# Kernel optimization log

Hardware: AMD Instinct MI355X
Metric: run time of the kernel (lower is better)

Reference implementation:

```python
import jax, jax.numpy as jnp
import numpy as np

DIM = 1024
HEADS = 16
DIM_HEAD = 64


def setup_inputs() -> dict:
    key = jax.random.key(0)
    ks = jax.random.split(key, 6)
    b, n = 2, 2048
    x = jax.random.normal(ks[0], (b, n, DIM), dtype=jnp.float32)
    gamma = jnp.ones((DIM,), dtype=jnp.float32)
    w_qkv = jax.random.normal(ks[1], (DIM, 3 * HEADS * DIM_HEAD), dtype=jnp.float32) * (DIM ** -0.5)
    w_gates = jax.random.normal(ks[2], (DIM, HEADS), dtype=jnp.float32) * (DIM ** -0.5)
    b_gates = jnp.zeros((HEADS,), dtype=jnp.float32)
    w_out = jax.random.normal(ks[3], (HEADS * DIM_HEAD, DIM), dtype=jnp.float32) * ((HEADS * DIM_HEAD) ** -0.5)
    freqs = jax.random.uniform(ks[4], (DIM_HEAD // 2,), dtype=jnp.float32)
    return {"x": x, "gamma": gamma, "w_qkv": w_qkv, "w_gates": w_gates,
            "b_gates": b_gates, "w_out": w_out, "freqs": freqs}


def _rotate_half(t):
    # interleaved pairs: (x1, x2) -> (-x2, x1)
    tp = t.reshape(t.shape[:-1] + (t.shape[-1] // 2, 2))
    x1, x2 = tp[..., 0], tp[..., 1]
    return jnp.stack((-x2, x1), axis=-1).reshape(t.shape)


def reference(x, gamma, w_qkv, w_gates, b_gates, w_out, freqs):
    b, n, d = x.shape
    # RMSNorm variant: divide by L2 norm, scale by gamma * sqrt(dim)
    xn = x / jnp.linalg.norm(x, axis=-1, keepdims=True)
    xn = xn * gamma * (d ** 0.5)
    # QKV projection: (b, n, 3*H*D) -> q,k,v each (b, h, n, dh)
    qkv = xn @ w_qkv
    qkv = qkv.reshape(b, n, 3, HEADS, DIM_HEAD).transpose(2, 0, 3, 1, 4)
    q, k, v = qkv[0], qkv[1], qkv[2]
    # Inline RoPE (interleaved): freqs (n, dh)
    pos = jnp.arange(n, dtype=freqs.dtype)
    f = jnp.repeat(pos[:, None] * freqs[None, :], 2, axis=-1)  # (n, dh)
    cos_f, sin_f = jnp.cos(f), jnp.sin(f)
    q = q * cos_f + _rotate_half(q) * sin_f
    k = k * cos_f + _rotate_half(k) * sin_f
    # SDPA
    scale = DIM_HEAD ** -0.5
    scores = jnp.einsum('bhqd,bhkd->bhqk', q, k) * scale
    attn = jax.nn.softmax(scores, axis=-1)
    out = jnp.einsum('bhqk,bhkd->bhqd', attn, v)  # (b, h, n, dh)
    # per-head sigmoid gate from normalized input
    gates = xn @ w_gates + b_gates  # (b, n, h)
    out = out * jax.nn.sigmoid(gates.transpose(0, 2, 1))[..., None]
    # merge heads and output projection
    out = out.transpose(0, 2, 1, 3).reshape(b, n, HEADS * DIM_HEAD)
    return out @ w_out
```

## Files before the change

kernel.cpp:

```cpp
#include <hip/hip_runtime.h>

typedef __bf16 bf16_t;
typedef __bf16 bf16x8 __attribute__((ext_vector_type(8)));
typedef __bf16 bf16x4 __attribute__((ext_vector_type(4)));
typedef float f32x4 __attribute__((ext_vector_type(4)));

#define B_  2
#define N_  2048
#define D_  1024
#define H_  16
#define DH_ 64

#define QSCALE 0.18033688011112042f
#define NEGC  -11.541560327111707f

#if __has_builtin(__builtin_amdgcn_exp2f)
#define EXP2F(x) __builtin_amdgcn_exp2f(x)
#else
#define EXP2F(x) exp2f(x)
#endif

#define GLL16(g, l) __builtin_amdgcn_global_load_lds( \
    (const __attribute__((address_space(1))) void*)(g), \
    (__attribute__((address_space(3))) void*)(l), 16, 0, 0)

__device__ __forceinline__ int xcd_swizzle_id() {
  int id = blockIdx.y * gridDim.x + blockIdx.x;
  int cpx = (gridDim.x * gridDim.y) >> 3;
  return (id & 7) * cpx + (id >> 3);
}

__global__ __launch_bounds__(256) void k_prep(
    const float* __restrict__ x, const float* __restrict__ gamma,
    const float* __restrict__ wg, const float* __restrict__ bg,
    bf16_t* __restrict__ xn, float* __restrict__ gsig,
    const float* __restrict__ w_qkv, bf16_t* __restrict__ wqkvT,
    const float* __restrict__ w_out, bf16_t* __restrict__ woutT,
    const float* __restrict__ freqs, float* __restrict__ tc, float* __restrict__ ts) {
  __shared__ __align__(16) char smem_raw[17424];
  int id = blockIdx.x, tid = threadIdx.x;
  if (id < 4096) {
    float* red4 = (float*)smem_raw;
    float (*red)[17] = (float(*)[17])(smem_raw + 16);
    int row = id;
    const float4* xr = (const float4*)(x + (size_t)row * D_);
    float4 v = xr[tid];
    float ss = v.x*v.x + v.y*v.y + v.z*v.z + v.w*v.w;
    #pragma unroll
    for (int off = 32; off > 0; off >>= 1) ss += __shfl_down(ss, off);
    if ((tid & 63) == 0) red4[tid >> 6] = ss;
    __syncthreads();
    float scale = 32.0f * rsqrtf(red4[0] + red4[1] + red4[2] + red4[3]);
    float4 g = ((const float4*)gamma)[tid];
    bf16x4 o;
    o[0] = (bf16_t)(v.x * scale * g.x);
    o[1] = (bf16_t)(v.y * scale * g.y);
    o[2] = (bf16_t)(v.z * scale * g.z);
    o[3] = (bf16_t)(v.w * scale * g.w);
    *(bf16x4*)(xn + (size_t)row * D_ + tid * 4) = o;
    float xv[4] = {(float)o[0], (float)o[1], (float)o[2], (float)o[3]};
    float part[16];
    #pragma unroll
    for (int h = 0; h < 16; ++h) part[h] = 0.f;
    #pragma unroll
    for (int j = 0; j < 4; ++j) {
      const float4* wr = (const float4*)&wg[(size_t)(tid * 4 + j) * 16];
      #pragma unroll
      for (int q = 0; q < 4; ++q) {
        float4 w4 = wr[q];
        part[q * 4 + 0] += xv[j] * w4.x;
        part[q * 4 + 1] += xv[j] * w4.y;
        part[q * 4 + 2] += xv[j] * w4.z;
        part[q * 4 + 3] += xv[j] * w4.w;
      }
    }
    #pragma unroll
    for (int h = 0; h < 16; ++h) red[tid][h] = part[h];
    __syncthreads();
    int h = tid & 15, grp = tid >> 4;
    float s = 0.f;
    #pragma unroll
    for (int k = 0; k < 16; ++k) s += red[grp * 16 + k][h];
    __syncthreads();
    red[grp][h] = s;
    __syncthreads();
    if (tid < 16) {
      float acc = bg[tid];
      #pragma unroll
      for (int k = 0; k < 16; ++k) acc += red[k][tid];
      gsig[(size_t)row * 16 + tid] = 1.0f / (1.0f + __expf(-acc));
    }
  } else if (id < 8192) {
    const float* W; bf16_t* Wt; int R, C, bx, by;
    if (id < 7168) { int local = id - 4096; W = w_qkv; Wt = wqkvT; R = 1024; C = 3072;
                     bx = local % 96; by = local / 96; }
    else           { int local = id - 7168; W = w_out; Wt = woutT; R = 1024; C = 1024;
                     bx = local & 31; by = local >> 5; }
    float (*tile)[33] = (float(*)[33])smem_raw;
    int c0 = bx * 32, r0 = by * 32;
    int tx = tid & 31, ty = tid >> 5;
    #pragma unroll
    for (int i = 0; i < 4; ++i) {
      int r = ty + i * 8;
      tile[r][tx] = W[(size_t)(r0 + r) * C + c0 + tx];
    }
    __syncthreads();
    #pragma unroll
    for (int i = 0; i < 4; ++i) {
      int rr = ty + i * 8;
      Wt[(size_t)(c0 + rr) * R + r0 + tx] = (bf16_t)tile[tx][rr];
    }
  } else {
    int idx = (id - 8192) * 256 + tid;
    int n = idx >> 5, j = idx & 31;
    float f = (float)n * freqs[j];
    tc[idx] = cosf(f);
    ts[idx] = sinf(f);
  }
}

__global__ __launch_bounds__(256) void k_gemm_qkv(const bf16_t* __restrict__ A,
    const bf16_t* __restrict__ Bt, const float* __restrict__ tc,
    const float* __restrict__ ts, bf16_t* __restrict__ Qb,
    bf16_t* __restrict__ Kb, bf16_t* __restrict__ Vb) {
  constexpr int BK = 32, K = 1024;
  constexpr int TP = 136;
  __shared__ __align__(16) char smem[128 * TP * 2];
  bf16_t* As0 = (bf16_t*)smem;
  bf16_t* Bs0 = (bf16_t*)(smem + 16384);
  bf16_t* Tt  = (bf16_t*)smem;
  int tid = threadIdx.x, wave = tid >> 6, lane = tid & 63;
  int l16 = lane & 15, quad = lane >> 4;
  int id = blockIdx.y * 32 + blockIdx.x;
  int xcd = id & 7, local = id >> 3;
  int bxi = (xcd & 3) * 8 + (local & 7);
  int byi = (xcd >> 2) * 12 + (local >> 3);
  int bm = bxi * 128, bn = byi * 128;
  int wm = (wave >> 1) * 64, wn = (wave & 1) * 64;
  int srow = wave * 32 + (lane >> 2);
  int scol = (lane & 3) * 8;
  const bf16_t* gA0 = &A [(size_t)(bm + srow)      * K + scol];
  const bf16_t* gA1 = &A [(size_t)(bm + srow + 16) * K + scol];
  const bf16_t* gB0 = &Bt[(size_t)(bn + srow)      * K + scol];
  const bf16_t* gB1 = &Bt[(size_t)(bn + srow + 16) * K + scol];
  bf16_t* lA0 = &As0[(wave * 32)      * BK];
  bf16_t* lA1 = &As0[(wave * 32 + 16) * BK];
  bf16_t* lB0 = &Bs0[(wave * 32)      * BK];
  bf16_t* lB1 = &Bs0[(wave * 32 + 16) * BK];
  f32x4 acc[4][4] = {};
  GLL16(gA0, lA0); GLL16(gA1, lA1); GLL16(gB0, lB0); GLL16(gB1, lB1);
  __syncthreads();
  for (int k0 = 0; k0 < K; k0 += BK) {
    int cur = (k0 >> 5) & 1;
    int co  = cur * 4096;
    int nxt = 4096 - co;
    if (k0 + BK < K) {
      GLL16(gA0 + k0 + BK, lA0 + nxt);
      GLL16(gA1 + k0 + BK, lA1 + nxt);
      GLL16(gB0 + k0 + BK, lB0 + nxt);
      GLL16(gB1 + k0 + BK, lB1 + nxt);
    }
    const bf16_t* Asc = As0 + co;
    const bf16_t* Bsc = Bs0 + co;
    bf16x8 af[4], bfr[4];
    #pragma unroll
    for (int t = 0; t < 4; ++t) {
      af[t]  = *(const bf16x8*)&Asc[(wm + t * 16 + l16) * BK + quad * 8];
      bfr[t] = *(const bf16x8*)&Bsc[(wn + t * 16 + l16) * BK + quad * 8];
    }
    #pragma unroll
    for (int mt = 0; mt < 4; ++mt)
      #pragma unroll
      for (int nt = 0; nt < 4; ++nt)
        acc[mt][nt] = __builtin_amdgcn_mfma_f32_16x16x32_bf16(af[mt], bfr[nt], acc[mt][nt], 0, 0, 0);
    __syncthreads();
  }
  if (byi < 16) {
    float qs = (byi < 8) ? QSCALE : 1.0f;
    bf16_t* dst = (byi < 8) ? Qb : Kb;
    #pragma unroll
    for (int mt = 0; mt < 4; ++mt)
      #pragma unroll
      for (int r = 0; r < 4; ++r) {
        int row_l = wm + mt * 16 + quad * 4 + r;
        int n = (bm + row_l) & 2047;
        const float* cr = tc + n * 32;
        const float* sr = ts + n * 32;
        #pragma unroll
        for (int nt = 0; nt < 4; ++nt) {
          int col_l = wn + nt * 16 + l16;
          int d = (bn + col_l) & 63, j = d >> 1;
          float val = acc[mt][nt][r];
          float p = __shfl_xor(val, 1);
          float c = cr[j], s = sr[j];
          float o = (d & 1) ? (val * c + p * s) : (val * c - p * s);
          Tt[row_l * TP + col_l] = (bf16_t)(o * qs);
        }
      }
    __syncthreads();
    #pragma unroll
    for (int it = 0; it < 8; ++it) {
      int idx = tid + 256 * it;
      int row_l = idx >> 4, ck = (idx & 15) * 8;
      bf16x8 v = *(const bf16x8*)&Tt[row_l * TP + ck];
      int grow = bm + row_l, b = grow >> 11, n = grow & 2047;
      int col = bn + ck, h = (col >> 6) & 15, d = col & 63;
      *(bf16x8*)&dst[((size_t)(b * H_ + h) * N_ + n) * DH_ + d] = v;
    }
  } else {
    #pragma unroll
    for (int mt = 0; mt < 4; ++mt)
      #pragma unroll
      for (int nt = 0; nt < 4; ++nt) {
        int col_l = wn + nt * 16 + l16;
        int row0 = wm + mt * 16 + quad * 4;
        #pragma unroll
        for (int r = 0; r < 4; ++r)
          Tt[col_l * TP + row0 + r] = (bf16_t)acc[mt][nt][r];
      }
    __syncthreads();
    int b = bm >> 11, nb = bm & 2047;
    #pragma unroll
    for (int it = 0; it < 8; ++it) {
      int idx = tid + 256 * it;
      int col_l = idx >> 4, ck = (idx & 15) * 8;
      bf16x8 v = *(const bf16x8*)&Tt[col_l * TP + ck];
      int vcol = bn + col_l - 2048, h = vcol >> 6, d = vcol & 63;
      *(bf16x8*)&Vb[((size_t)(b * H_ + h) * DH_ + d) * N_ + nb + ck] = v;
    }
  }
}

__global__ __launch_bounds__(256) void k_gemm_bt_n64(const bf16_t* __restrict__ A,
    const bf16_t* __restrict__ Bt, float* __restrict__ C, int M, int N, int K) {
  constexpr int BK = 32;
  __shared__ __align__(16) bf16_t As0[128 * BK * 2];
  __shared__ __align__(16) bf16_t Bs0[64 * BK * 2];
  int tid = threadIdx.x, wave = tid >> 6, lane = tid & 63;
  int l16 = lane & 15, quad = lane >> 4;
  int id = blockIdx.y * 32 + blockIdx.x;
  int xcd = id & 7, local = id >> 3;
  int bxi = (xcd & 3) * 8 + (local & 7);
  int byi = (xcd >> 2) * 8 + (local >> 3);
  int bm = bxi * 128, bn = byi * 64;
  int wm = (wave >> 1) * 64, wn = (wave & 1) * 32;
  int srow = wave * 32 + (lane >> 2);
  int scol = (lane & 3) * 8;
  const bf16_t* gA0 = &A [(size_t)(bm + srow)      * K + scol];
  const bf16_t* gA1 = &A [(size_t)(bm + srow + 16) * K + scol];
  int srB = wave * 16 + (lane >> 2);
  const bf16_t* gB0 = &Bt[(size_t)(bn + srB) * K + scol];
  bf16_t* lA0 = &As0[(wave * 32)      * BK];
  bf16_t* lA1 = &As0[(wave * 32 + 16) * BK];
  bf16_t* lB0 = &Bs0[(wave * 16)      * BK];
  f32x4 acc[4][2] = {};
  GLL16(gA0, lA0); GLL16(gA1, lA1); GLL16(gB0, lB0);
  __syncthreads();
  for (int k0 = 0; k0 < K; k0 += BK) {
    int cur = (k0 >> 5) & 1;
    int coA = cur * 4096, nxA = 4096 - coA;
    int coB = cur * 2048, nxB = 2048 - coB;
    if (k0 + BK < K) {
      GLL16(gA0 + k0 + BK, lA0 + nxA);
      GLL16(gA1 + k0 + BK, lA1 + nxA);
      GLL16(gB0 + k0 + BK, lB0 + nxB);
    }
    const bf16_t* Asc = As0 + coA;
    const bf16_t* Bsc = Bs0 + coB;
    bf16x8 af[4], bfr[2];
    #pragma unroll
    for (int t = 0; t < 4; ++t)
      af[t]  = *(const bf16x8*)&Asc[(wm + t * 16 + l16) * BK + quad * 8];
    #pragma unroll
    for (int t = 0; t < 2; ++t)
      bfr[t] = *(const bf16x8*)&Bsc[(wn + t * 16 + l16) * BK + quad * 8];
    #pragma unroll
    for (int mt = 0; mt < 4; ++mt)
      #pragma unroll
      for (int nt = 0; nt < 2; ++nt)
        acc[mt][nt] = __builtin_amdgcn_mfma_f32_16x16x32_bf16(af[mt], bfr[nt], acc[mt][nt], 0, 0, 0);
    __syncthreads();
  }
  #pragma unroll
  for (int mt = 0; mt < 4; ++mt)
    #pragma unroll
    for (int nt = 0; nt < 2; ++nt)
      #pragma unroll
      for (int r = 0; r < 4; ++r) {
        int row = bm + wm + mt * 16 + quad * 4 + r;
        int col = bn + wn + nt * 16 + l16;
        C[(size_t)row * N + col] = acc[mt][nt][r];
      }
}

__global__ __launch_bounds__(256) void k_flash(const bf16_t* __restrict__ Qb,
    const bf16_t* __restrict__ Kb, const bf16_t* __restrict__ Vb,
    const float* __restrict__ gsig, bf16_t* __restrict__ Ao) {
  __shared__ __align__(16) bf16_t Ks[2][64 * 72];
  __shared__ __align__(16) bf16_t Vt[2][64 * 72];
  __shared__ __align__(16) bf16_t Ps[4][32 * 72];
  int swz = xcd_swizzle_id();
  int qblk = swz & 15, bh = swz >> 4;
  int b = bh >> 4, h = bh & 15;
  int tid = threadIdx.x, wave = tid >> 6, lane = tid & 63;
  int l16 = lane & 15, quad = lane >> 4;
  int qw = qblk * 128 + wave * 32;
  const bf16_t* Qh = Qb + (size_t)bh * N_ * DH_;
  const bf16_t* Kh = Kb + (size_t)bh * N_ * DH_;
  const bf16_t* Vh = Vb + (size_t)bh * DH_ * N_;
  bf16_t* Pw = Ps[wave];
  bf16x8 qf[2][2];
  #pragma unroll
  for (int qt = 0; qt < 2; ++qt)
    #pragma unroll
    for (int hf = 0; hf < 2; ++hf)
      qf[qt][hf] = *(const bf16x8*)&Qh[(size_t)(qw + qt * 16 + l16) * DH_ + hf * 32 + quad * 8];
  bf16x8 onesf;
  #pragma unroll
  for (int i = 0; i < 8; ++i) onesf[i] = (bf16_t)1.0f;
  f32x4 accO[2][4] = {};
  f32x4 accL[2] = {};
  int sk = tid >> 3;
  int sc = (tid & 7) * 8;
  bf16x8 rk0 = *(const bf16x8*)&Kh[(size_t)sk * DH_ + sc];
  bf16x8 rk1 = *(const bf16x8*)&Kh[(size_t)(sk + 32) * DH_ + sc];
  bf16x8 rv0 = *(const bf16x8*)&Vh[(size_t)sk * N_ + sc];
  bf16x8 rv1 = *(const bf16x8*)&Vh[(size_t)(sk + 32) * N_ + sc];
  *(bf16x8*)&Ks[0][sk * 72 + sc]        = rk0;
  *(bf16x8*)&Ks[0][(sk + 32) * 72 + sc] = rk1;
  *(bf16x8*)&Vt[0][sk * 72 + sc]        = rv0;
  *(bf16x8*)&Vt[0][(sk + 32) * 72 + sc] = rv1;
  __syncthreads();
  const f32x4 zinit = {NEGC, NEGC, NEGC, NEGC};
  for (int k0 = 0; k0 < N_; k0 += 64) {
    int cur = (k0 >> 6) & 1;
    const bf16_t* Kc = Ks[cur];
    const bf16_t* Vc = Vt[cur];
    int kn = k0 + 64;
    if (kn < N_) {
      rk0 = *(const bf16x8*)&Kh[(size_t)(kn + sk) * DH_ + sc];
      rk1 = *(const bf16x8*)&Kh[(size_t)(kn + sk + 32) * DH_ + sc];
      rv0 = *(const bf16x8*)&Vh[(size_t)sk * N_ + kn + sc];
      rv1 = *(const bf16x8*)&Vh[(size_t)(sk + 32) * N_ + kn + sc];
    }
    f32x4 st[4][2];
    __builtin_amdgcn_s_setprio(1);
    #pragma unroll
    for (int kt = 0; kt < 4; ++kt) {
      bf16x8 kf0 = *(const bf16x8*)&Kc[(kt * 16 + l16) * 72 + quad * 8];
      bf16x8 kf1 = *(const bf16x8*)&Kc[(kt * 16 + l16) * 72 + 32 + quad * 8];
      #pragma unroll
      for (int qt = 0; qt < 2; ++qt) {
        f32x4 z = zinit;
        z = __builtin_amdgcn_mfma_f32_16x16x32_bf16(kf0, qf[qt][0], z, 0, 0, 0);
        z = __builtin_amdgcn_mfma_f32_16x16x32_bf16(kf1, qf[qt][1], z, 0, 0, 0);
        st[kt][qt] = z;
      }
    }
    __builtin_amdgcn_s_setprio(0);
    #pragma unroll
    for (int qt = 0; qt < 2; ++qt)
      #pragma unroll
      for (int kt = 0; kt < 4; ++kt) {
        bf16x4 pk;
        #pragma unroll
        for (int r = 0; r < 4; ++r)
          pk[r] = (bf16_t)EXP2F(st[kt][qt][r]);
        *(bf16x4*)&Pw[(qt * 16 + l16) * 72 + kt * 16 + quad * 4] = pk;
      }
    bf16x8 pf[2][2];
    #pragma unroll
    for (int qt = 0; qt < 2; ++qt)
      #pragma unroll
      for (int hf = 0; hf < 2; ++hf)
        pf[qt][hf] = *(const bf16x8*)&Pw[(qt * 16 + l16) * 72 + hf * 32 + quad * 8];
    __builtin_amdgcn_s_setprio(1);
    #pragma unroll
    for (int qt = 0; qt < 2; ++qt) {
      accL[qt] = __builtin_amdgcn_mfma_f32_16x16x32_bf16(pf[qt][0], onesf, accL[qt], 0, 0, 0);
      accL[qt] = __builtin_amdgcn_mfma_f32_16x16x32_bf16(pf[qt][1], onesf, accL[qt], 0, 0, 0);
    }
    #pragma unroll
    for (int dt = 0; dt < 4; ++dt)
      #pragma unroll
      for (int hf = 0; hf < 2; ++hf) {
        bf16x8 vf = *(const bf16x8*)&Vc[(dt * 16 + l16) * 72 + hf * 32 + quad * 8];
        #pragma unroll
        for (int qt = 0; qt < 2; ++qt)
          accO[qt][dt] = __builtin_amdgcn_mfma_f32_16x16x32_bf16(pf[qt][hf], vf, accO[qt][dt], 0, 0, 0);
      }
    __builtin_amdgcn_s_setprio(0);
    if (kn < N_) {
      int nb = cur ^ 1;
      *(bf16x8*)&Ks[nb][sk * 72 + sc]        = rk0;
      *(bf16x8*)&Ks[nb][(sk + 32) * 72 + sc] = rk1;
      *(bf16x8*)&Vt[nb][sk * 72 + sc]        = rv0;
      *(bf16x8*)&Vt[nb][(sk + 32) * 72 + sc] = rv1;
    }
    __syncthreads();
  }
  #pragma unroll
  for (int qt = 0; qt < 2; ++qt)
    #pragma unroll
    for (int r = 0; r < 4; ++r) {
      int q = qw + qt * 16 + quad * 4 + r;
      float g = gsig[((size_t)b * N_ + q) * H_ + h];
      float ginv = g / accL[qt][r];
      #pragma unroll
      for (int dt = 0; dt < 4; ++dt)
        Ao[((size_t)b * N_ + q) * (H_ * DH_) + h * DH_ + dt * 16 + l16] =
            (bf16_t)(accO[qt][dt][r] * ginv);
    }
}

extern "C" void kernel_launch(void* const* d_in, const int* in_sizes, int n_in,
                              void* d_out, int out_size, void* d_ws, size_t ws_size,
                              hipStream_t stream) {
  (void)in_sizes; (void)n_in; (void)out_size; (void)ws_size;
  const float* x      = (const float*)d_in[0];
  const float* gamma  = (const float*)d_in[1];
  const float* w_qkv  = (const float*)d_in[2];
  const float* w_gate = (const float*)d_in[3];
  const float* b_gate = (const float*)d_in[4];
  const float* w_out  = (const float*)d_in[5];
  const float* freqs  = (const float*)d_in[6];
  float* out = (float*)d_out;
  char* ws = (char*)d_ws;
  bf16_t* xn    = (bf16_t*)(ws);
  bf16_t* wqkvT = (bf16_t*)(ws + ((size_t)8  << 20));
  bf16_t* woutT = (bf16_t*)(ws + ((size_t)14 << 20));
  bf16_t* Qb    = (bf16_t*)(ws + ((size_t)16 << 20));
  bf16_t* Kb    = (bf16_t*)(ws + ((size_t)24 << 20));
  bf16_t* Vb    = (bf16_t*)(ws + ((size_t)32 << 20));
  float*  gsig  = (float*) (ws + ((size_t)40 << 20));
  bf16_t* attn  = (bf16_t*)(ws + ((size_t)41 << 20));
  float*  trigc = (float*) (ws + ((size_t)49 << 20));
  float*  trigs = (float*) (ws + ((size_t)50 << 20));

  k_prep<<<8448, 256, 0, stream>>>(x, gamma, w_gate, b_gate, xn, gsig,
                                   w_qkv, wqkvT, w_out, woutT, freqs, trigc, trigs);
  k_gemm_qkv<<<dim3(32, 24), 256, 0, stream>>>(xn, wqkvT, trigc, trigs, Qb, Kb, Vb);
  k_flash<<<dim3(16, 32), 256, 0, stream>>>(Qb, Kb, Vb, gsig, attn);
  k_gemm_bt_n64<<<dim3(32, 16), 256, 0, stream>>>(attn, woutT, out, 4096, 1024, 1024);
}
```

Measured before the change: 219.8 us.

## Load K and V fragments directly from global memory in flash kernel

```diff
diff --git a/kernel.cpp b/kernel.cpp
--- a/kernel.cpp
+++ b/kernel.cpp
@@ -296,8 +296,6 @@
 __global__ __launch_bounds__(256) void k_flash(const bf16_t* __restrict__ Qb,
     const bf16_t* __restrict__ Kb, const bf16_t* __restrict__ Vb,
     const float* __restrict__ gsig, bf16_t* __restrict__ Ao) {
-  __shared__ __align__(16) bf16_t Ks[2][64 * 72];
-  __shared__ __align__(16) bf16_t Vt[2][64 * 72];
   __shared__ __align__(16) bf16_t Ps[4][32 * 72];
   int swz = xcd_swizzle_id();
   int qblk = swz & 15, bh = swz >> 4;
@@ -320,44 +318,34 @@
   for (int i = 0; i < 8; ++i) onesf[i] = (bf16_t)1.0f;
   f32x4 accO[2][4] = {};
   f32x4 accL[2] = {};
-  int sk = tid >> 3;
-  int sc = (tid & 7) * 8;
-  bf16x8 rk0 = *(const bf16x8*)&Kh[(size_t)sk * DH_ + sc];
-  bf16x8 rk1 = *(const bf16x8*)&Kh[(size_t)(sk + 32) * DH_ + sc];
-  bf16x8 rv0 = *(const bf16x8*)&Vh[(size_t)sk * N_ + sc];
-  bf16x8 rv1 = *(const bf16x8*)&Vh[(size_t)(sk + 32) * N_ + sc];
-  *(bf16x8*)&Ks[0][sk * 72 + sc]        = rk0;
-  *(bf16x8*)&Ks[0][(sk + 32) * 72 + sc] = rk1;
-  *(bf16x8*)&Vt[0][sk * 72 + sc]        = rv0;
-  *(bf16x8*)&Vt[0][(sk + 32) * 72 + sc] = rv1;
-  __syncthreads();
+  bf16x8 kf[4][2];
+  #pragma unroll
+  for (int kt = 0; kt < 4; ++kt) {
+    kf[kt][0] = *(const bf16x8*)&Kh[(size_t)(kt * 16 + l16) * DH_ + quad * 8];
+    kf[kt][1] = *(const bf16x8*)&Kh[(size_t)(kt * 16 + l16) * DH_ + 32 + quad * 8];
+  }
   const f32x4 zinit = {NEGC, NEGC, NEGC, NEGC};
   for (int k0 = 0; k0 < N_; k0 += 64) {
-    int cur = (k0 >> 6) & 1;
-    const bf16_t* Kc = Ks[cur];
-    const bf16_t* Vc = Vt[cur];
+    f32x4 st[4][2];
+    __builtin_amdgcn_s_setprio(1);
+    #pragma unroll
+    for (int kt = 0; kt < 4; ++kt)
+      #pragma unroll
+      for (int qt = 0; qt < 2; ++qt) {
+        f32x4 z = zinit;
+        z = __builtin_amdgcn_mfma_f32_16x16x32_bf16(kf[kt][0], qf[qt][0], z, 0, 0, 0);
+        z = __builtin_amdgcn_mfma_f32_16x16x32_bf16(kf[kt][1], qf[qt][1], z, 0, 0, 0);
+        st[kt][qt] = z;
+      }
+    __builtin_amdgcn_s_setprio(0);
     int kn = k0 + 64;
     if (kn < N_) {
-      rk0 = *(const bf16x8*)&Kh[(size_t)(kn + sk) * DH_ + sc];
-      rk1 = *(const bf16x8*)&Kh[(size_t)(kn + sk + 32) * DH_ + sc];
-      rv0 = *(const bf16x8*)&Vh[(size_t)sk * N_ + kn + sc];
-      rv1 = *(const bf16x8*)&Vh[(size_t)(sk + 32) * N_ + kn + sc];
-    }
-    f32x4 st[4][2];
-    __builtin_amdgcn_s_setprio(1);
-    #pragma unroll
-    for (int kt = 0; kt < 4; ++kt) {
-      bf16x8 kf0 = *(const bf16x8*)&Kc[(kt * 16 + l16) * 72 + quad * 8];
-      bf16x8 kf1 = *(const bf16x8*)&Kc[(kt * 16 + l16) * 72 + 32 + quad * 8];
-      #pragma unroll
-      for (int qt = 0; qt < 2; ++qt) {
-        f32x4 z = zinit;
-        z = __builtin_amdgcn_mfma_f32_16x16x32_bf16(kf0, qf[qt][0], z, 0, 0, 0);
-        z = __builtin_amdgcn_mfma_f32_16x16x32_bf16(kf1, qf[qt][1], z, 0, 0, 0);
-        st[kt][qt] = z;
-      }
-    }
-    __builtin_amdgcn_s_setprio(0);
+      #pragma unroll
+      for (int kt = 0; kt < 4; ++kt) {
+        kf[kt][0] = *(const bf16x8*)&Kh[(size_t)(kn + kt * 16 + l16) * DH_ + quad * 8];
+        kf[kt][1] = *(const bf16x8*)&Kh[(size_t)(kn + kt * 16 + l16) * DH_ + 32 + quad * 8];
+      }
+    }
     #pragma unroll
     for (int qt = 0; qt < 2; ++qt)
       #pragma unroll
@@ -384,20 +372,12 @@
     for (int dt = 0; dt < 4; ++dt)
       #pragma unroll
       for (int hf = 0; hf < 2; ++hf) {
-        bf16x8 vf = *(const bf16x8*)&Vc[(dt * 16 + l16) * 72 + hf * 32 + quad * 8];
+        bf16x8 vf = *(const bf16x8*)&Vh[(size_t)(dt * 16 + l16) * N_ + k0 + hf * 32 + quad * 8];
         #pragma unroll
         for (int qt = 0; qt < 2; ++qt)
           accO[qt][dt] = __builtin_amdgcn_mfma_f32_16x16x32_bf16(pf[qt][hf], vf, accO[qt][dt], 0, 0, 0);
       }
     __builtin_amdgcn_s_setprio(0);
-    if (kn < N_) {
-      int nb = cur ^ 1;
-      *(bf16x8*)&Ks[nb][sk * 72 + sc]        = rk0;
-      *(bf16x8*)&Ks[nb][(sk + 32) * 72 + sc] = rk1;
-      *(bf16x8*)&Vt[nb][sk * 72 + sc]        = rv0;
-      *(bf16x8*)&Vt[nb][(sk + 32) * 72 + sc] = rv1;
-    }
-    __syncthreads();
   }
   #pragma unroll
   for (int qt = 0; qt < 2; ++qt)
```

After: 288.0 us. +31.0%, slower.
